# Optimization experiments

Hardware: AMD Instinct MI355X
Metric: run time of the kernel (lower is better)

Reference implementation:

```python
import jax, jax.numpy as jnp
import numpy as np

N = 100000        # nodes
E = 1600000       # edges (N * avg_degree 16)
D_IN = 128
D_OUT = 32
OBS_T = 60        # observation_time -> decay table size 60*OBS_T = 3600
T_MAX = 60 * OBS_T


def setup_inputs() -> dict:
    key = jax.random.key(0)
    ks = jax.random.split(key, 8)
    inp = {
        "input": jax.random.normal(ks[0], (N, D_IN), dtype=jnp.float32),
        "W": jax.random.normal(ks[1], (D_IN, D_OUT), dtype=jnp.float32) * (np.sqrt(2.0) / np.sqrt(D_IN)),
        # decay weights are abs(normal(0, 0.02)) in the original; rand*0.04 is same scale
        "decay_weight1": jnp.abs(jax.random.normal(ks[2], (T_MAX, 1), dtype=jnp.float32) * 0.02),
        "decay_weight2": jnp.abs(jax.random.normal(ks[3], (T_MAX, 1), dtype=jnp.float32) * 0.02),
        "edge_row": jax.random.randint(ks[4], (E,), 0, N, dtype=jnp.int32),
        "edge_col": jax.random.randint(ks[5], (E,), 0, N, dtype=jnp.int32),
        # zero-based interval index; equals (adj_value - 1) of the original code
        "edge_time": jax.random.randint(ks[6], (E,), 0, T_MAX, dtype=jnp.int32),
        "arrive_time": jax.random.randint(ks[7], (N,), 0, T_MAX, dtype=jnp.int32),
        "observation_time": OBS_T,
    }
    return inp


def reference(input, W, decay_weight1, decay_weight2,
              edge_row, edge_col, edge_time, arrive_time, observation_time):
    n_nodes = input.shape[0]
    # h = relu(input @ W)  [N, D_OUT]
    h = jax.nn.relu(jnp.matmul(input, W))
    # one-hot(interval) @ decay_weight1 == embedding lookup  -> per-edge decay scalar
    decay = decay_weight1[edge_time, 0]                        # [E]
    # SpecialSpmm: out[i] = sum_{edges (i,j)} decay_e * h[j]  (gather-scale-scatter)
    msgs = decay[:, None] * h[edge_col]                        # [E, D_OUT]
    h_prime = jax.ops.segment_sum(msgs, edge_row, num_segments=n_nodes)
    # outlayer window decay: one-hot(60*T - arrive - 1) @ decay_weight2 == lookup
    win_idx = 60 * observation_time - arrive_time - 1          # [N] in [0, 60*T)
    h_prime = decay_weight2[win_idx, 0][:, None] * h_prime
    return h_prime
```

## Files before the change

kernel.cpp:

```cpp
#include <hip/hip_runtime.h>

#define N_NODES 100000
#define N_EDGES 1600000
#define D_IN    128
#define D_OUT   32
#define CROWS   2048
#define NCB     49
#define NSH     8
#define NSEG    (NCB * NSH)
#define CAP_A   4500
#define DEPTH   48
#define SEGSTRIDE 4608
#define SSTRIDE 2064
#define CAPW    1024
#define RPB3    32
#define K3_BLKS (NCB * 64)
#define GEMM_BLKS ((N_NODES + 63) / 64)
#define GRID_A  2048
#define EPB_A   ((N_EDGES + GRID_A - 1) / GRID_A)

typedef __attribute__((ext_vector_type(8))) short bf16x8;
typedef __attribute__((ext_vector_type(4))) float f32x4;

__device__ inline short f2bf(float f) {
    union { float f; unsigned u; } v; v.f = f;
    unsigned r = (v.u + 0x7FFFu + ((v.u >> 16) & 1u)) >> 16;
    return (short)r;
}

__global__ __launch_bounds__(256) void phaseA_kernel(
    const int* __restrict__ erow,    const int* __restrict__ ecol,
    const int* __restrict__ etime,
    int* __restrict__ gcur,
    uint2* __restrict__ segA)
{
    __shared__ struct { uint2 lbin[NCB][DEPTH]; int lcnt[NCB]; int gbase[NCB]; } sm;
    const int tid = threadIdx.x;

    const int blk   = blockIdx.x;
    const int shard = blk & (NSH - 1);
    const int wv    = tid >> 6;
    const int ln    = tid & 63;

    if (tid < NCB) sm.lcnt[tid] = 0;
    __syncthreads();

    const int e_beg = blk * EPB_A;
    const int e_end = min(e_beg + EPB_A, N_EDGES);

    for (int e = e_beg + tid; e < e_end; e += 256) {
        const int row = erow[e];
        const int cb  = row >> 11;
        uint2 p;
        p.x = (unsigned)ecol[e] | ((unsigned)(row & (CROWS - 1)) << 17);
        p.y = (unsigned)etime[e];
        const int pos = atomicAdd(&sm.lcnt[cb], 1);
        if (pos < DEPTH) sm.lbin[cb][pos] = p;
        else {
            const int gp = atomicAdd(&gcur[(cb * NSH + shard) * 16], 1);
            if (gp < CAP_A) segA[(size_t)(cb * NSH + shard) * CAP_A + gp] = p;
        }
    }
    __syncthreads();

    if (tid < NCB) {
        const int c = min(sm.lcnt[tid], DEPTH);
        sm.gbase[tid] = atomicAdd(&gcur[(tid * NSH + shard) * 16], c);
    }
    __syncthreads();

    for (int bin = wv; bin < NCB; bin += 4) {
        const int c  = min(sm.lcnt[bin], DEPTH);
        const int gb = sm.gbase[bin];
        uint2* seg = segA + (size_t)(bin * NSH + shard) * CAP_A;
        for (int k = ln; k < c; k += 64)
            if (gb + k < CAP_A) seg[gb + k] = sm.lbin[bin][k];
    }
}

union SMemGS {
    struct { short wbt[D_IN * D_OUT]; } g;
    struct { int hist[CROWS]; int curs[CROWS]; int part[256]; } s;
};

__global__ __launch_bounds__(256) void gemm_sortseg_kernel(
    const float* __restrict__ input, const float* __restrict__ W,
    unsigned short* __restrict__ h16,
    const int* __restrict__ gcur, const uint2* __restrict__ segA,
    int* __restrict__ sseg, unsigned* __restrict__ spk2s)
{
    __shared__ SMemGS sm;
    const int tid = threadIdx.x;

    if (blockIdx.x < NSEG) {
        const int b = blockIdx.x;
        const int n = min(gcur[b * 16], CAP_A);
        const uint2* seg = segA + (size_t)b * CAP_A;

        for (int t = tid; t < CROWS; t += 256) sm.s.hist[t] = 0;
        __syncthreads();

        for (int i = tid; i < n; i += 256)
            atomicAdd(&sm.s.hist[(seg[i].x >> 17) & (CROWS - 1)], 1);
        __syncthreads();

        int tmp[8]; int s0 = 0;
        const int base = tid * 8;
#pragma unroll
        for (int k = 0; k < 8; ++k) { tmp[k] = sm.s.hist[base + k]; s0 += tmp[k]; }
        sm.s.part[tid] = s0;
        __syncthreads();
        for (int off = 1; off < 256; off <<= 1) {
            int v = sm.s.part[tid];
            if (tid >= off) v += sm.s.part[tid - off];
            __syncthreads(); sm.s.part[tid] = v; __syncthreads();
        }
        int run = sm.s.part[tid] - s0;
#pragma unroll
        for (int k = 0; k < 8; ++k) { sm.s.curs[base + k] = run; run += tmp[k]; }
        __syncthreads();

        int* sg = sseg + (size_t)b * SSTRIDE;
        for (int t = tid; t < CROWS; t += 256) sg[t] = sm.s.curs[t];
        if (tid == 0) sg[CROWS] = n;
        __syncthreads();

        unsigned* dst = spk2s + (size_t)b * SEGSTRIDE;
        for (int i = tid; i < n; i += 256) {
            const uint2 p  = seg[i];
            const int   rl = (p.x >> 17) & (CROWS - 1);
            dst[atomicAdd(&sm.s.curs[rl], 1)] = (p.x & 0x1FFFFu) | (p.y << 20);
        }
    } else {
        const int gblk = blockIdx.x - NSEG;
        for (int i = tid; i < D_IN * D_OUT; i += 256) {
            const int k = i >> 5, c = i & 31;
            sm.g.wbt[c * D_IN + k] = f2bf(W[i]);
        }
        __syncthreads();

        const int wave = tid >> 6;
        const int lane = tid & 63;
        const int r0   = gblk * 64 + wave * 16;
        const int c16  = lane & 15;
        const int quad = lane >> 4;

        int ra = r0 + c16;
        if (ra >= N_NODES) ra = N_NODES - 1;
        const float* arow = input + (size_t)ra * D_IN;

        f32x4 acc0 = {0.f, 0.f, 0.f, 0.f};
        f32x4 acc1 = {0.f, 0.f, 0.f, 0.f};
#pragma unroll
        for (int q = 0; q < 4; ++q) {
            const float* ap = arow + q * 32 + quad * 8;
            f32x4 a0 = *(const f32x4*)(ap);
            f32x4 a1 = *(const f32x4*)(ap + 4);
            bf16x8 af;
            af[0] = f2bf(a0.x); af[1] = f2bf(a0.y); af[2] = f2bf(a0.z); af[3] = f2bf(a0.w);
            af[4] = f2bf(a1.x); af[5] = f2bf(a1.y); af[6] = f2bf(a1.z); af[7] = f2bf(a1.w);
            bf16x8 b0 = *(const bf16x8*)(sm.g.wbt + (c16)      * D_IN + q * 32 + quad * 8);
            bf16x8 b1 = *(const bf16x8*)(sm.g.wbt + (c16 + 16) * D_IN + q * 32 + quad * 8);
            acc0 = __builtin_amdgcn_mfma_f32_16x16x32_bf16(af, b0, acc0, 0, 0, 0);
            acc1 = __builtin_amdgcn_mfma_f32_16x16x32_bf16(af, b1, acc1, 0, 0, 0);
        }
#pragma unroll
        for (int i = 0; i < 4; ++i) {
            const int rr = r0 + quad * 4 + i;
            if (rr < N_NODES) {
                h16[(size_t)rr * D_OUT + c16]      = (unsigned short)f2bf(fmaxf(acc0[i], 0.f));
                h16[(size_t)rr * D_OUT + c16 + 16] = (unsigned short)f2bf(fmaxf(acc1[i], 0.f));
            }
        }
    }
}

__global__ __launch_bounds__(256) void merge_reduce_kernel(
    const unsigned short* __restrict__ h16, const int* __restrict__ sseg,
    const unsigned* __restrict__ spk2s,
    const float* __restrict__ dw1, const float* __restrict__ dw2,
    const int* __restrict__ arrive, const int* __restrict__ obs,
    float* __restrict__ out)
{
    __shared__ int ls8[NSH][RPB3 + 1];
    __shared__ int pre[NSH][RPB3];
    __shared__ int totL[RPB3];
    __shared__ int dstart[RPB3 + 1];
    __shared__ unsigned st[CAPW];

    const int b   = blockIdx.x;
    const int cb  = b >> 6;
    const int rl0 = (b & 63) * RPB3;
    const int g0  = cb * CROWS + rl0;
    if (g0 >= N_NODES) return;
    const int tid = threadIdx.x;

    for (int t = tid; t < NSH * (RPB3 + 1); t += 256) {
        const int s = t / (RPB3 + 1), i = t - s * (RPB3 + 1);
        ls8[s][i] = sseg[(size_t)(cb * NSH + s) * SSTRIDE + rl0 + i];
    }
    __syncthreads();

    if (tid < RPB3) {
        int accp = 0;
#pragma unroll
        for (int s = 0; s < NSH; ++s) {
            pre[s][tid] = accp;
            accp += ls8[s][tid + 1] - ls8[s][tid];
        }
        totL[tid] = accp;
    }
    __syncthreads();
    if (tid == 0) {
        int runp = 0;
#pragma unroll
        for (int r = 0; r < RPB3; ++r) { dstart[r] = runp; runp += totL[r]; }
        dstart[RPB3] = runp;
    }
    __syncthreads();

#pragma unroll
    for (int s = 0; s < NSH; ++s) {
        const int sb   = ls8[s][0];
        const int span = ls8[s][RPB3] - sb;
        const unsigned* src = spk2s + (size_t)(cb * NSH + s) * SEGSTRIDE;
        for (int i = tid; i < span; i += 256) {
            const int gidx = sb + i;
            int lo = 0, hi = RPB3 - 1;
#pragma unroll
            for (int it = 0; it < 5; ++it) {
                const int mid = (lo + hi + 1) >> 1;
                if (ls8[s][mid] <= gidx) lo = mid; else hi = mid - 1;
            }
            const int pos = dstart[lo] + pre[s][lo] + (gidx - ls8[s][lo]);
            if (pos < CAPW) st[pos] = src[gidx];
        }
    }
    __syncthreads();

    const int g  = tid >> 3;
    const int li = tid & 7;
    const int row = g0 + g;
    const int begc = min(dstart[g], CAPW);
    const int endc = min(dstart[g + 1], CAPW);
    const int n    = endc - begc;
    const unsigned* recs = &st[begc];
    const unsigned short* hp = h16 + li * 4;

    float a0 = 0.f, a1 = 0.f, a2 = 0.f, a3 = 0.f;
    int j = 0;
    for (; j + 8 <= n; j += 8) {
#pragma unroll
        for (int u = 0; u < 8; ++u) {
            const unsigned rec = recs[j + u];
            const uint2 hv = *(const uint2*)(hp + ((size_t)(rec & 0x1FFFFu) << 5));
            const float w  = dw1[rec >> 20];
            a0 = fmaf(w, __uint_as_float(hv.x << 16),         a0);
            a1 = fmaf(w, __uint_as_float(hv.x & 0xFFFF0000u), a1);
            a2 = fmaf(w, __uint_as_float(hv.y << 16),         a2);
            a3 = fmaf(w, __uint_as_float(hv.y & 0xFFFF0000u), a3);
        }
    }
    for (; j < n; ++j) {
        const unsigned rec = recs[j];
        const uint2 hv = *(const uint2*)(hp + ((size_t)(rec & 0x1FFFFu) << 5));
        const float w  = dw1[rec >> 20];
        a0 = fmaf(w, __uint_as_float(hv.x << 16),         a0);
        a1 = fmaf(w, __uint_as_float(hv.x & 0xFFFF0000u), a1);
        a2 = fmaf(w, __uint_as_float(hv.y << 16),         a2);
        a3 = fmaf(w, __uint_as_float(hv.y & 0xFFFF0000u), a3);
    }

    const int T = 60 * obs[0];
    const float sdw = dw2[T - arrive[row] - 1];
    float4 o;
    o.x = a0 * sdw; o.y = a1 * sdw; o.z = a2 * sdw; o.w = a3 * sdw;
    *(float4*)(out + ((size_t)row << 5) + li * 4) = o;
}

extern "C" void kernel_launch(void* const* d_in, const int* in_sizes, int n_in,
                              void* d_out, int out_size, void* d_ws, size_t ws_size,
                              hipStream_t stream)
{
    const float* input  = (const float*)d_in[0];
    const float* W      = (const float*)d_in[1];
    const float* dw1    = (const float*)d_in[2];
    const float* dw2    = (const float*)d_in[3];
    const int*   erow   = (const int*)d_in[4];
    const int*   ecol   = (const int*)d_in[5];
    const int*   etime  = (const int*)d_in[6];
    const int*   arrive = (const int*)d_in[7];
    const int*   obs    = (const int*)d_in[8];

    float* out = (float*)d_out;

    char* p = (char*)d_ws;
    unsigned short* h16 = (unsigned short*)p;
    p += (size_t)N_NODES * D_OUT * 2;
    p = (char*)(((size_t)p + 255) & ~(size_t)255);
    int* gcur = (int*)p;
    p += (size_t)NSEG * 16 * 4;
    p = (char*)(((size_t)p + 255) & ~(size_t)255);
    uint2* segA = (uint2*)p;
    p += (size_t)NSEG * CAP_A * 8;
    p = (char*)(((size_t)p + 255) & ~(size_t)255);
    unsigned* spk2s = (unsigned*)p;
    p += (size_t)NSEG * SEGSTRIDE * 4;
    p = (char*)(((size_t)p + 255) & ~(size_t)255);
    int* sseg = (int*)p;

    hipMemsetAsync(gcur, 0, (size_t)NSEG * 16 * 4, stream);

    phaseA_kernel<<<GRID_A, 256, 0, stream>>>(erow, ecol, etime, gcur, segA);
    gemm_sortseg_kernel<<<NSEG + GEMM_BLKS, 256, 0, stream>>>(
        input, W, h16, gcur, segA, sseg, spk2s);
    merge_reduce_kernel<<<K3_BLKS, 256, 0, stream>>>(
        h16, sseg, spk2s, dw1, dw2, arrive, obs, out);
}
```

Measured before the change: 179.0 us.

## Split GEMM blocks between edge-binning and segment-sort kernels to balance load

The dense GEMM work that computes h is split into two parts. About half the GEMM blocks now run in the same launch as the edge-binning pass, and the rest stay with the per-segment sort pass. The goal is to balance the two launches so the GEMM work hides behind the binning and sort work, which are bound by memory traffic and atomics. In exchange, shared memory is now a union across both roles, which can limit occupancy, and the split point is a fixed constant.

Result: no change. 176.2 us (-1.5%).

```diff
diff --git a/kernel.cpp b/kernel.cpp
--- a/kernel.cpp
+++ b/kernel.cpp
@@ -16,6 +16,8 @@
 #define RPB3    32
 #define K3_BLKS (NCB * 64)
 #define GEMM_BLKS ((N_NODES + 63) / 64)
+#define GEMM_A  782
+#define GEMM_B  (GEMM_BLKS - GEMM_A)
 #define GRID_A  2048
 #define EPB_A   ((N_EDGES + GRID_A - 1) / GRID_A)
 
@@ -28,68 +30,125 @@
     return (short)r;
 }
 
-__global__ __launch_bounds__(256) void phaseA_kernel(
+__device__ inline void gemm_role(const float* __restrict__ input,
+                                 const float* __restrict__ W,
+                                 unsigned short* __restrict__ h16,
+                                 short* wbt, int gblk, int tid)
+{
+    for (int i = tid; i < D_IN * D_OUT; i += 256) {
+        const int k = i >> 5, c = i & 31;
+        wbt[c * D_IN + k] = f2bf(W[i]);
+    }
+    __syncthreads();
+
+    const int wave = tid >> 6;
+    const int lane = tid & 63;
+    const int r0   = gblk * 64 + wave * 16;
+    const int c16  = lane & 15;
+    const int quad = lane >> 4;
+
+    int ra = r0 + c16;
+    if (ra >= N_NODES) ra = N_NODES - 1;
+    const float* arow = input + (size_t)ra * D_IN;
+
+    f32x4 acc0 = {0.f, 0.f, 0.f, 0.f};
+    f32x4 acc1 = {0.f, 0.f, 0.f, 0.f};
+#pragma unroll
+    for (int q = 0; q < 4; ++q) {
+        const float* ap = arow + q * 32 + quad * 8;
+        f32x4 a0 = *(const f32x4*)(ap);
+        f32x4 a1 = *(const f32x4*)(ap + 4);
+        bf16x8 af;
+        af[0] = f2bf(a0.x); af[1] = f2bf(a0.y); af[2] = f2bf(a0.z); af[3] = f2bf(a0.w);
+        af[4] = f2bf(a1.x); af[5] = f2bf(a1.y); af[6] = f2bf(a1.z); af[7] = f2bf(a1.w);
+        bf16x8 b0 = *(const bf16x8*)(wbt + (c16)      * D_IN + q * 32 + quad * 8);
+        bf16x8 b1 = *(const bf16x8*)(wbt + (c16 + 16) * D_IN + q * 32 + quad * 8);
+        acc0 = __builtin_amdgcn_mfma_f32_16x16x32_bf16(af, b0, acc0, 0, 0, 0);
+        acc1 = __builtin_amdgcn_mfma_f32_16x16x32_bf16(af, b1, acc1, 0, 0, 0);
+    }
+#pragma unroll
+    for (int i = 0; i < 4; ++i) {
+        const int rr = r0 + quad * 4 + i;
+        if (rr < N_NODES) {
+            h16[(size_t)rr * D_OUT + c16]      = (unsigned short)f2bf(fmaxf(acc0[i], 0.f));
+            h16[(size_t)rr * D_OUT + c16 + 16] = (unsigned short)f2bf(fmaxf(acc1[i], 0.f));
+        }
+    }
+}
+
+union SMemPAG {
+    struct { uint2 lbin[NCB][DEPTH]; int lcnt[NCB]; int gbase[NCB]; } a;
+    struct { short wbt[D_IN * D_OUT]; } g;
+};
+
+__global__ __launch_bounds__(256) void phaseA_gemmA_kernel(
+    const float* __restrict__ input, const float* __restrict__ W,
     const int* __restrict__ erow,    const int* __restrict__ ecol,
     const int* __restrict__ etime,
+    unsigned short* __restrict__ h16,
     int* __restrict__ gcur,
     uint2* __restrict__ segA)
 {
-    __shared__ struct { uint2 lbin[NCB][DEPTH]; int lcnt[NCB]; int gbase[NCB]; } sm;
+    __shared__ SMemPAG sm;
     const int tid = threadIdx.x;
 
-    const int blk   = blockIdx.x;
-    const int shard = blk & (NSH - 1);
-    const int wv    = tid >> 6;
-    const int ln    = tid & 63;
-
-    if (tid < NCB) sm.lcnt[tid] = 0;
-    __syncthreads();
-
-    const int e_beg = blk * EPB_A;
-    const int e_end = min(e_beg + EPB_A, N_EDGES);
-
-    for (int e = e_beg + tid; e < e_end; e += 256) {
-        const int row = erow[e];
-        const int cb  = row >> 11;
-        uint2 p;
-        p.x = (unsigned)ecol[e] | ((unsigned)(row & (CROWS - 1)) << 17);
-        p.y = (unsigned)etime[e];
-        const int pos = atomicAdd(&sm.lcnt[cb], 1);
-        if (pos < DEPTH) sm.lbin[cb][pos] = p;
-        else {
-            const int gp = atomicAdd(&gcur[(cb * NSH + shard) * 16], 1);
-            if (gp < CAP_A) segA[(size_t)(cb * NSH + shard) * CAP_A + gp] = p;
-        }
-    }
-    __syncthreads();
-
-    if (tid < NCB) {
-        const int c = min(sm.lcnt[tid], DEPTH);
-        sm.gbase[tid] = atomicAdd(&gcur[(tid * NSH + shard) * 16], c);
-    }
-    __syncthreads();
-
-    for (int bin = wv; bin < NCB; bin += 4) {
-        const int c  = min(sm.lcnt[bin], DEPTH);
-        const int gb = sm.gbase[bin];
-        uint2* seg = segA + (size_t)(bin * NSH + shard) * CAP_A;
-        for (int k = ln; k < c; k += 64)
-            if (gb + k < CAP_A) seg[gb + k] = sm.lbin[bin][k];
-    }
-}
-
-union SMemGS {
+    if (blockIdx.x < GRID_A) {
+        const int blk   = blockIdx.x;
+        const int shard = blk & (NSH - 1);
+        const int wv    = tid >> 6;
+        const int ln    = tid & 63;
+
+        if (tid < NCB) sm.a.lcnt[tid] = 0;
+        __syncthreads();
+
+        const int e_beg = blk * EPB_A;
+        const int e_end = min(e_beg + EPB_A, N_EDGES);
+
+        for (int e = e_beg + tid; e < e_end; e += 256) {
+            const int row = erow[e];
+            const int cb  = row >> 11;
+            uint2 p;
+            p.x = (unsigned)ecol[e] | ((unsigned)(row & (CROWS - 1)) << 17);
+            p.y = (unsigned)etime[e];
+            const int pos = atomicAdd(&sm.a.lcnt[cb], 1);
+            if (pos < DEPTH) sm.a.lbin[cb][pos] = p;
+            else {
+                const int gp = atomicAdd(&gcur[(cb * NSH + shard) * 16], 1);
+                if (gp < CAP_A) segA[(size_t)(cb * NSH + shard) * CAP_A + gp] = p;
+            }
+        }
+        __syncthreads();
+
+        if (tid < NCB) {
+            const int c = min(sm.a.lcnt[tid], DEPTH);
+            sm.a.gbase[tid] = atomicAdd(&gcur[(tid * NSH + shard) * 16], c);
+        }
+        __syncthreads();
+
+        for (int bin = wv; bin < NCB; bin += 4) {
+            const int c  = min(sm.a.lcnt[bin], DEPTH);
+            const int gb = sm.a.gbase[bin];
+            uint2* seg = segA + (size_t)(bin * NSH + shard) * CAP_A;
+            for (int k = ln; k < c; k += 64)
+                if (gb + k < CAP_A) seg[gb + k] = sm.a.lbin[bin][k];
+        }
+    } else {
+        gemm_role(input, W, h16, sm.g.wbt, blockIdx.x - GRID_A, tid);
+    }
+}
+
+union SMemSSG {
+    struct { int hist[CROWS]; int curs[CROWS]; int part[256]; } s;
     struct { short wbt[D_IN * D_OUT]; } g;
-    struct { int hist[CROWS]; int curs[CROWS]; int part[256]; } s;
 };
 
-__global__ __launch_bounds__(256) void gemm_sortseg_kernel(
+__global__ __launch_bounds__(256) void sortseg_gemmB_kernel(
     const float* __restrict__ input, const float* __restrict__ W,
     unsigned short* __restrict__ h16,
     const int* __restrict__ gcur, const uint2* __restrict__ segA,
     int* __restrict__ sseg, unsigned* __restrict__ spk2s)
 {
-    __shared__ SMemGS sm;
+    __shared__ SMemSSG sm;
     const int tid = threadIdx.x;
 
     if (blockIdx.x < NSEG) {
@@ -132,46 +191,7 @@
             dst[atomicAdd(&sm.s.curs[rl], 1)] = (p.x & 0x1FFFFu) | (p.y << 20);
         }
     } else {
-        const int gblk = blockIdx.x - NSEG;
-        for (int i = tid; i < D_IN * D_OUT; i += 256) {
-            const int k = i >> 5, c = i & 31;
-            sm.g.wbt[c * D_IN + k] = f2bf(W[i]);
-        }
-        __syncthreads();
-
-        const int wave = tid >> 6;
-        const int lane = tid & 63;
-        const int r0   = gblk * 64 + wave * 16;
-        const int c16  = lane & 15;
-        const int quad = lane >> 4;
-
-        int ra = r0 + c16;
-        if (ra >= N_NODES) ra = N_NODES - 1;
-        const float* arow = input + (size_t)ra * D_IN;
-
-        f32x4 acc0 = {0.f, 0.f, 0.f, 0.f};
-        f32x4 acc1 = {0.f, 0.f, 0.f, 0.f};
-#pragma unroll
-        for (int q = 0; q < 4; ++q) {
-            const float* ap = arow + q * 32 + quad * 8;
-            f32x4 a0 = *(const f32x4*)(ap);
-            f32x4 a1 = *(const f32x4*)(ap + 4);
-            bf16x8 af;
-            af[0] = f2bf(a0.x); af[1] = f2bf(a0.y); af[2] = f2bf(a0.z); af[3] = f2bf(a0.w);
-            af[4] = f2bf(a1.x); af[5] = f2bf(a1.y); af[6] = f2bf(a1.z); af[7] = f2bf(a1.w);
-            bf16x8 b0 = *(const bf16x8*)(sm.g.wbt + (c16)      * D_IN + q * 32 + quad * 8);
-            bf16x8 b1 = *(const bf16x8*)(sm.g.wbt + (c16 + 16) * D_IN + q * 32 + quad * 8);
-            acc0 = __builtin_amdgcn_mfma_f32_16x16x32_bf16(af, b0, acc0, 0, 0, 0);
-            acc1 = __builtin_amdgcn_mfma_f32_16x16x32_bf16(af, b1, acc1, 0, 0, 0);
-        }
-#pragma unroll
-        for (int i = 0; i < 4; ++i) {
-            const int rr = r0 + quad * 4 + i;
-            if (rr < N_NODES) {
-                h16[(size_t)rr * D_OUT + c16]      = (unsigned short)f2bf(fmaxf(acc0[i], 0.f));
-                h16[(size_t)rr * D_OUT + c16 + 16] = (unsigned short)f2bf(fmaxf(acc1[i], 0.f));
-            }
-        }
+        gemm_role(input, W, h16, sm.g.wbt, GEMM_A + (int)blockIdx.x - NSEG, tid);
     }
 }
 
@@ -311,8 +331,9 @@
 
     hipMemsetAsync(gcur, 0, (size_t)NSEG * 16 * 4, stream);
 
-    phaseA_kernel<<<GRID_A, 256, 0, stream>>>(erow, ecol, etime, gcur, segA);
-    gemm_sortseg_kernel<<<NSEG + GEMM_BLKS, 256, 0, stream>>>(
+    phaseA_gemmA_kernel<<<GRID_A + GEMM_A, 256, 0, stream>>>(
+        input, W, erow, ecol, etime, h16, gcur, segA);
+    sortseg_gemmB_kernel<<<NSEG + GEMM_B, 256, 0, stream>>>(
         input, W, h16, gcur, segA, sseg, spk2s);
     merge_reduce_kernel<<<K3_BLKS, 256, 0, stream>>>(
         h16, sseg, spk2s, dw1, dw2, arrive, obs, out);
```
